# Kernel tuning notes

Hardware: AMD Instinct MI355X
Metric: run time of the kernel (lower is better)

## Reference

```python
import jax, jax.numpy as jnp
import numpy as np

N, M, P = 64, 64, 64
T = 262144

def setup_inputs() -> dict:
    key = jax.random.key(0)
    ks = jax.random.split(key, 6)
    return {
        "u": jax.random.normal(ks[0], (T, M), dtype=jnp.float32),
        "x0": jax.random.normal(ks[1], (N,), dtype=jnp.float32),
        "A": jax.random.normal(ks[2], (N, N), dtype=jnp.float32) * 0.1,
        "B": jax.random.normal(ks[3], (N, M), dtype=jnp.float32) * 0.1,
        "C": jax.random.normal(ks[4], (P, N), dtype=jnp.float32) * 0.1,
        "D": jax.random.normal(ks[5], (P, M), dtype=jnp.float32) * 0.1,
    }

def reference(u, x0, A, B, C, D):
    # Precompute input drives in one big GEMM each: Bu[k] = B @ u[k], Du[k] = D @ u[k]
    Bu = u @ B.T            # (T, n)
    Du = u @ D.T            # (T, p)

    def step(x, bu):
        # y_k uses pre-update state x_k; next state x_{k+1} = A x_k + B u_k
        x_next = A @ x + bu
        return x_next, x     # carry new state, emit x_k

    _, xs = jax.lax.scan(step, x0, Bu)   # xs: (T, n) = [x_0 ... x_{T-1}]
    ys = xs @ C.T + Du                   # (T, p)
    return ys
```

## Files before the change

### kernel.cpp

```cpp
#include <hip/hip_runtime.h>


#define T_LEN  262144
#define NTAP   33
#define ZLEN   48
#define ROWS   512
#define HALO   32

typedef __attribute__((ext_vector_type(8))) short  short8;
typedef __attribute__((ext_vector_type(4))) short  short4v;
typedef __attribute__((ext_vector_type(4))) float  floatx4;

static __device__ __forceinline__ unsigned short f2bf(float f) {
    unsigned int x = __float_as_uint(f);
    x += 0x7fffu + ((x >> 16) & 1u);
    return (unsigned short)(x >> 16);
}
static __device__ __forceinline__ float bf2f(unsigned short u) {
    return __uint_as_float(((unsigned int)u) << 16);
}

__global__ __launch_bounds__(256, 1) void k_prep(
    const float* __restrict__ A, const float* __restrict__ B,
    const float* __restrict__ C, const float* __restrict__ D,
    const float* __restrict__ x0, unsigned short* __restrict__ gG,
    float* __restrict__ gZ)
{
    __shared__ unsigned short pool[10][64][72];
    const int tid = threadIdx.x;
    const int wv = tid >> 6, lane = tid & 63, l15 = lane & 15, q = lane >> 4;

#pragma unroll
    for (int e = 0; e < 16; ++e) {
        int f = e * 256 + tid;
        int r = f >> 6, c = f & 63;
        unsigned short av = f2bf(A[f]);
        pool[0][r][c] = av;
        pool[1][c][r] = av;
        pool[2][c][r] = f2bf(B[f]);
        pool[6][r][c] = f2bf(C[f]);
        gG[f]         = f2bf(D[f]);
    }
    __syncthreads();

    float x0v[4];
#pragma unroll
    for (int nt = 0; nt < 4; ++nt) x0v[nt] = x0[l15 + 16 * nt];

    {
        short8 bA[2][4];
#pragma unroll
        for (int kb = 0; kb < 2; ++kb)
#pragma unroll
            for (int nt = 0; nt < 4; ++nt)
                bA[kb][nt] = *(const short8*)&pool[1][l15 + 16*nt][kb*32 + q*8];

        short8 a0 = *(const short8*)&pool[0][16*wv + l15][q*8];
        short8 a1 = *(const short8*)&pool[0][16*wv + l15][32 + q*8];
#pragma unroll
        for (int nt = 0; nt < 4; ++nt) {
            floatx4 m = (floatx4){0.f, 0.f, 0.f, 0.f};
            m = __builtin_amdgcn_mfma_f32_16x16x32_bf16(a0, bA[0][nt], m, 0, 0, 0);
            m = __builtin_amdgcn_mfma_f32_16x16x32_bf16(a1, bA[1][nt], m, 0, 0, 0);
#pragma unroll
            for (int r = 0; r < 4; ++r) {
                unsigned short h = f2bf(m[r]);
                pool[3][16*wv + q*4 + r][l15 + 16*nt] = h;
                pool[4][l15 + 16*nt][16*wv + q*4 + r] = h;
            }
        }
        a0 = *(const short8*)&pool[6][16*wv + l15][q*8];
        a1 = *(const short8*)&pool[6][16*wv + l15][32 + q*8];
#pragma unroll
        for (int nt = 0; nt < 4; ++nt) {
            floatx4 m = (floatx4){0.f, 0.f, 0.f, 0.f};
            m = __builtin_amdgcn_mfma_f32_16x16x32_bf16(a0, bA[0][nt], m, 0, 0, 0);
            m = __builtin_amdgcn_mfma_f32_16x16x32_bf16(a1, bA[1][nt], m, 0, 0, 0);
#pragma unroll
            for (int r = 0; r < 4; ++r)
                pool[7][16*wv + q*4 + r][l15 + 16*nt] = f2bf(m[r]);
        }
    }
    __syncthreads();

    {
        short8 bA2[2][4];
#pragma unroll
        for (int kb = 0; kb < 2; ++kb)
#pragma unroll
            for (int nt = 0; nt < 4; ++nt)
                bA2[kb][nt] = *(const short8*)&pool[4][l15 + 16*nt][kb*32 + q*8];

        short8 a0 = *(const short8*)&pool[3][16*wv + l15][q*8];
        short8 a1 = *(const short8*)&pool[3][16*wv + l15][32 + q*8];
#pragma unroll
        for (int nt = 0; nt < 4; ++nt) {
            floatx4 m = (floatx4){0.f, 0.f, 0.f, 0.f};
            m = __builtin_amdgcn_mfma_f32_16x16x32_bf16(a0, bA2[0][nt], m, 0, 0, 0);
            m = __builtin_amdgcn_mfma_f32_16x16x32_bf16(a1, bA2[1][nt], m, 0, 0, 0);
#pragma unroll
            for (int r = 0; r < 4; ++r)
                pool[5][l15 + 16*nt][16*wv + q*4 + r] = f2bf(m[r]);
        }
        a0 = *(const short8*)&pool[6][16*wv + l15][q*8];
        a1 = *(const short8*)&pool[6][16*wv + l15][32 + q*8];
#pragma unroll
        for (int nt = 0; nt < 4; ++nt) {
            floatx4 m = (floatx4){0.f, 0.f, 0.f, 0.f};
            m = __builtin_amdgcn_mfma_f32_16x16x32_bf16(a0, bA2[0][nt], m, 0, 0, 0);
            m = __builtin_amdgcn_mfma_f32_16x16x32_bf16(a1, bA2[1][nt], m, 0, 0, 0);
#pragma unroll
            for (int r = 0; r < 4; ++r)
                pool[8][16*wv + q*4 + r][l15 + 16*nt] = f2bf(m[r]);
        }
        a0 = *(const short8*)&pool[7][16*wv + l15][q*8];
        a1 = *(const short8*)&pool[7][16*wv + l15][32 + q*8];
#pragma unroll
        for (int nt = 0; nt < 4; ++nt) {
            floatx4 m = (floatx4){0.f, 0.f, 0.f, 0.f};
            m = __builtin_amdgcn_mfma_f32_16x16x32_bf16(a0, bA2[0][nt], m, 0, 0, 0);
            m = __builtin_amdgcn_mfma_f32_16x16x32_bf16(a1, bA2[1][nt], m, 0, 0, 0);
#pragma unroll
            for (int r = 0; r < 4; ++r)
                pool[9][16*wv + q*4 + r][l15 + 16*nt] = f2bf(m[r]);
        }
    }
    __syncthreads();

    short8 bE[2][4], bB[2][4];
#pragma unroll
    for (int kb = 0; kb < 2; ++kb)
#pragma unroll
        for (int nt = 0; nt < 4; ++nt) {
            bE[kb][nt] = *(const short8*)&pool[5][l15 + 16*nt][kb*32 + q*8];
            bB[kb][nt] = *(const short8*)&pool[2][l15 + 16*nt][kb*32 + q*8];
        }
    __syncthreads();

    unsigned short (*cur)[72] = pool[6 + wv];
    unsigned short (*alt)[72] = pool[wv];

#pragma unroll
    for (int mt = 0; mt < 4; ++mt)
#pragma unroll
        for (int r = 0; r < 4; ++r) {
            float v = 0.f;
#pragma unroll
            for (int nt = 0; nt < 4; ++nt)
                v += bf2f(cur[16*mt + q*4 + r][l15 + 16*nt]) * x0v[nt];
            v += __shfl_xor(v, 1, 16); v += __shfl_xor(v, 2, 16);
            v += __shfl_xor(v, 4, 16); v += __shfl_xor(v, 8, 16);
            if (l15 == 0) gZ[wv*64 + 16*mt + q*4 + r] = v;
        }

    for (int k = 1; k <= 11; ++k) {
        const int jm = 4*(k-1) + wv;
        short8 a0[4], a1[4];
#pragma unroll
        for (int mt = 0; mt < 4; ++mt) {
            a0[mt] = *(const short8*)&cur[16*mt + l15][q*8];
            a1[mt] = *(const short8*)&cur[16*mt + l15][32 + q*8];
        }
        if (jm < 32) {
#pragma unroll
            for (int mt = 0; mt < 4; ++mt)
#pragma unroll
                for (int nt = 0; nt < 4; ++nt) {
                    floatx4 g = (floatx4){0.f, 0.f, 0.f, 0.f};
                    g = __builtin_amdgcn_mfma_f32_16x16x32_bf16(a0[mt], bB[0][nt], g, 0, 0, 0);
                    g = __builtin_amdgcn_mfma_f32_16x16x32_bf16(a1[mt], bB[1][nt], g, 0, 0, 0);
#pragma unroll
                    for (int r = 0; r < 4; ++r)
                        gG[(size_t)(jm+1)*4096 + (16*mt + q*4 + r)*64 + l15 + 16*nt] = f2bf(g[r]);
                }
        }
        floatx4 m[4][4];
#pragma unroll
        for (int mt = 0; mt < 4; ++mt)
#pragma unroll
            for (int nt = 0; nt < 4; ++nt) {
                m[mt][nt] = (floatx4){0.f, 0.f, 0.f, 0.f};
                m[mt][nt] = __builtin_amdgcn_mfma_f32_16x16x32_bf16(a0[mt], bE[0][nt], m[mt][nt], 0, 0, 0);
                m[mt][nt] = __builtin_amdgcn_mfma_f32_16x16x32_bf16(a1[mt], bE[1][nt], m[mt][nt], 0, 0, 0);
            }
#pragma unroll
        for (int mt = 0; mt < 4; ++mt)
#pragma unroll
            for (int nt = 0; nt < 4; ++nt)
#pragma unroll
                for (int r = 0; r < 4; ++r)
                    alt[16*mt + q*4 + r][l15 + 16*nt] = f2bf(m[mt][nt][r]);
        const int zi = 4*k + wv;
#pragma unroll
        for (int mt = 0; mt < 4; ++mt)
#pragma unroll
            for (int r = 0; r < 4; ++r) {
                float v = 0.f;
#pragma unroll
                for (int nt = 0; nt < 4; ++nt) v = fmaf(m[mt][nt][r], x0v[nt], v);
                v += __shfl_xor(v, 1, 16); v += __shfl_xor(v, 2, 16);
                v += __shfl_xor(v, 4, 16); v += __shfl_xor(v, 8, 16);
                if (l15 == 0) gZ[zi*64 + 16*mt + q*4 + r] = v;
            }
        unsigned short (*tmp)[72] = cur; cur = alt; alt = tmp;
    }
}

__global__ __launch_bounds__(512, 2) void k_conv(
    const float* __restrict__ u, const unsigned short* __restrict__ gG,
    const float* __restrict__ gZ, float* __restrict__ out)
{
    __shared__ __align__(16) unsigned char uS[(ROWS + HALO) * 128];
    const int tid = threadIdx.x;
    const int wv = tid >> 6, lane = tid & 63, l15 = lane & 15, q = lane >> 4;
    const int nhalf = wv & 1, rg = wv >> 1;
    const int t0 = blockIdx.x * ROWS;

    {
        const float4* u4 = (const float4*)u;
        const int base4 = (t0 - HALO) * 16;
#pragma unroll
        for (int e = 0; e < 17; ++e) {
            int f = e * 512 + tid;
            float4 v = make_float4(0.f, 0.f, 0.f, 0.f);
            if (base4 + f >= 0) v = u4[base4 + f];
            int r  = f >> 4;
            int cb = (f & 15) * 8;
            short4v pk;
            pk[0] = (short)f2bf(v.x); pk[1] = (short)f2bf(v.y);
            pk[2] = (short)f2bf(v.z); pk[3] = (short)f2bf(v.w);
            *(short4v*)(uS + (r * 128 + (cb ^ ((r & 7) << 4)))) = pk;
        }
    }
    __syncthreads();

    floatx4 acc[8][2];
#pragma unroll
    for (int mt = 0; mt < 8; ++mt)
#pragma unroll
        for (int nt = 0; nt < 2; ++nt) acc[mt][nt] = (floatx4){0.f, 0.f, 0.f, 0.f};

    auto loadG2 = [&](short8 (&c0)[2][2], short8 (&c1)[2][2], int j) {
#pragma unroll
        for (int kb = 0; kb < 2; ++kb)
#pragma unroll
            for (int nt = 0; nt < 2; ++nt) {
                const size_t off = (size_t)(l15 + 16*(2*nhalf + nt))*64 + kb*32 + q*8;
                c1[kb][nt] = *(const short8*)(gG + (size_t)(j + 16)*4096 + off);
                c0[kb][nt] = *(const short8*)(gG + (size_t)j*4096 + off);
            }
    };
    auto sweep = [&](const short8 (&c0)[2][2], const short8 (&c1)[2][2], int j) {
        const int swz  = ((l15 - j) & 7) << 4;
        const int rowb = (rg*128 + 16 - j + l15) * 128;
        const int cb0 = (q * 16) ^ swz;
        const int cb1 = (64 + q * 16) ^ swz;
        short8 av[9], bv[9];
#pragma unroll
        for (int rt = 0; rt <= 8; ++rt)
            av[rt] = *(const short8*)(uS + (rowb + rt * 2048 + cb0));
#pragma unroll
        for (int rt = 0; rt <= 8; ++rt)
            bv[rt] = *(const short8*)(uS + (rowb + rt * 2048 + cb1));
#pragma unroll
        for (int rt = 0; rt <= 8; ++rt) {
            if (rt >= 1) {
#pragma unroll
                for (int nt = 0; nt < 2; ++nt)
                    acc[rt-1][nt] = __builtin_amdgcn_mfma_f32_16x16x32_bf16(
                        av[rt], c0[0][nt], acc[rt-1][nt], 0, 0, 0);
            }
            if (rt <= 7) {
#pragma unroll
                for (int nt = 0; nt < 2; ++nt)
                    acc[rt][nt] = __builtin_amdgcn_mfma_f32_16x16x32_bf16(
                        av[rt], c1[0][nt], acc[rt][nt], 0, 0, 0);
            }
        }
#pragma unroll
        for (int rt = 0; rt <= 8; ++rt) {
            if (rt >= 1) {
#pragma unroll
                for (int nt = 0; nt < 2; ++nt)
                    acc[rt-1][nt] = __builtin_amdgcn_mfma_f32_16x16x32_bf16(
                        bv[rt], c0[1][nt], acc[rt-1][nt], 0, 0, 0);
            }
            if (rt <= 7) {
#pragma unroll
                for (int nt = 0; nt < 2; ++nt)
                    acc[rt][nt] = __builtin_amdgcn_mfma_f32_16x16x32_bf16(
                        bv[rt], c1[1][nt], acc[rt][nt], 0, 0, 0);
            }
        }
    };

    short8 bA0[2][2], bA1[2][2], bB0[2][2], bB1[2][2];
    loadG2(bA0, bA1, 0);
#pragma unroll 1
    for (int jj = 0; jj < 8; ++jj) {
        loadG2(bB0, bB1, 2*jj + 1);
        sweep(bA0, bA1, 2*jj);
        if (jj < 7) loadG2(bA0, bA1, 2*jj + 2);
        sweep(bB0, bB1, 2*jj + 1);
    }

    {
        short8 bt[2][2];
#pragma unroll
        for (int kb = 0; kb < 2; ++kb)
#pragma unroll
            for (int nt = 0; nt < 2; ++nt)
                bt[kb][nt] = *(const short8*)(gG + (size_t)32*4096
                                  + (size_t)(l15 + 16*(2*nhalf + nt))*64 + kb*32 + q*8);
        const int swz  = (l15 & 7) << 4;
        const int rowb = (rg*128 + l15) * 128;
        const int cb0 = (q * 16) ^ swz;
        const int cb1 = (64 + q * 16) ^ swz;
        short8 av[8], bv[8];
#pragma unroll
        for (int mt = 0; mt < 8; ++mt)
            av[mt] = *(const short8*)(uS + (rowb + mt * 2048 + cb0));
#pragma unroll
        for (int mt = 0; mt < 8; ++mt)
            bv[mt] = *(const short8*)(uS + (rowb + mt * 2048 + cb1));
#pragma unroll
        for (int mt = 0; mt < 8; ++mt)
#pragma unroll
            for (int nt = 0; nt < 2; ++nt)
                acc[mt][nt] = __builtin_amdgcn_mfma_f32_16x16x32_bf16(
                    av[mt], bt[0][nt], acc[mt][nt], 0, 0, 0);
#pragma unroll
        for (int mt = 0; mt < 8; ++mt)
#pragma unroll
            for (int nt = 0; nt < 2; ++nt)
                acc[mt][nt] = __builtin_amdgcn_mfma_f32_16x16x32_bf16(
                    bv[mt], bt[1][nt], acc[mt][nt], 0, 0, 0);
    }

    const bool zblk = (blockIdx.x == 0 && rg == 0);
#pragma unroll
    for (int mt = 0; mt < 8; ++mt)
#pragma unroll
        for (int nt = 0; nt < 2; ++nt) {
            const int p = l15 + 32*nhalf + 16*nt;
#pragma unroll
            for (int r = 0; r < 4; ++r) {
                int tl = rg*128 + mt*16 + q*4 + r;
                float v = acc[mt][nt][r];
                if (zblk && mt < 3) v += gZ[(mt*16 + q*4 + r)*64 + p];
                out[(size_t)(t0 + tl)*64 + p] = v;
            }
        }
}

extern "C" void kernel_launch(void* const* d_in, const int* in_sizes, int n_in,
                              void* d_out, int out_size, void* d_ws, size_t ws_size,
                              hipStream_t stream) {
    const float* u  = (const float*)d_in[0];
    const float* x0 = (const float*)d_in[1];
    const float* A  = (const float*)d_in[2];
    const float* B  = (const float*)d_in[3];
    const float* C  = (const float*)d_in[4];
    const float* D  = (const float*)d_in[5];
    float* out = (float*)d_out;

    unsigned short* gG = (unsigned short*)d_ws;
    float* gZ = (float*)((char*)d_ws + 272384);

    hipLaunchKernelGGL(k_prep, dim3(1), dim3(256), 0, stream,
                       A, B, C, D, x0, gG, gZ);
    hipLaunchKernelGGL(k_conv, dim3(T_LEN / ROWS), dim3(512), 0, stream,
                       u, gG, gZ, out);
}
```

Baseline: 239.4 us.

## Pre-cast input to bf16 buffer and read operands directly from global memory

Adds a separate cast kernel that converts u to a zero-padded bf16 buffer in the workspace, then a new convolution kernel that reads MFMA operands straight from this buffer through the cache instead of staging fp32 input into swizzled LDS. Block size drops to 256 threads covering 256 rows. The aim is to remove the LDS staging and the fp32-to-bf16 conversion from the main kernel. In exchange it adds an extra launch plus a full write and re-read of a bf16 copy of u, and the halo rows are now loaded redundantly from global memory. The old LDS path remains as a fallback when the workspace is too small.

```diff
diff --git a/kernel.cpp b/kernel.cpp
--- a/kernel.cpp
+++ b/kernel.cpp
@@ -4,8 +4,8 @@
 #define T_LEN  262144
 #define NTAP   33
 #define ZLEN   48
-#define ROWS   512
 #define HALO   32
+#define UB_ROWS (T_LEN + HALO)
 
 typedef __attribute__((ext_vector_type(8))) short  short8;
 typedef __attribute__((ext_vector_type(4))) short  short4v;
@@ -18,6 +18,24 @@
 }
 static __device__ __forceinline__ float bf2f(unsigned short u) {
     return __uint_as_float(((unsigned int)u) << 16);
+}
+
+__global__ __launch_bounds__(256) void k_cast(
+    const float* __restrict__ u, unsigned short* __restrict__ uB)
+{
+    const size_t e8 = ((size_t)blockIdx.x * 256 + threadIdx.x) * 8;
+    short8 pk;
+    if (e8 < (size_t)HALO * 64) {
+        pk = (short8){0, 0, 0, 0, 0, 0, 0, 0};
+    } else {
+        const float4* s = (const float4*)(u + (e8 - (size_t)HALO * 64));
+        float4 v0 = s[0], v1 = s[1];
+        pk[0] = (short)f2bf(v0.x); pk[1] = (short)f2bf(v0.y);
+        pk[2] = (short)f2bf(v0.z); pk[3] = (short)f2bf(v0.w);
+        pk[4] = (short)f2bf(v1.x); pk[5] = (short)f2bf(v1.y);
+        pk[6] = (short)f2bf(v1.z); pk[7] = (short)f2bf(v1.w);
+    }
+    *(short8*)(uB + e8) = pk;
 }
 
 __global__ __launch_bounds__(256, 1) void k_prep(
@@ -206,7 +224,136 @@
     }
 }
 
-__global__ __launch_bounds__(512, 2) void k_conv(
+__global__ __launch_bounds__(256, 2) void k_conv_g(
+    const unsigned short* __restrict__ uB, const unsigned short* __restrict__ gG,
+    const float* __restrict__ gZ, float* __restrict__ out)
+{
+    const int tid = threadIdx.x;
+    const int wv = tid >> 6, lane = tid & 63, l15 = lane & 15, q = lane >> 4;
+    const int nhalf = wv & 1, rg = wv >> 1;
+    const int t0 = blockIdx.x * 256;
+    const unsigned char* uBb = (const unsigned char*)uB;
+
+    floatx4 acc[8][2];
+#pragma unroll
+    for (int mt = 0; mt < 8; ++mt)
+#pragma unroll
+        for (int nt = 0; nt < 2; ++nt) acc[mt][nt] = (floatx4){0.f, 0.f, 0.f, 0.f};
+
+    auto loadG2 = [&](short8 (&c0)[2][2], short8 (&c1)[2][2], int j) {
+#pragma unroll
+        for (int kb = 0; kb < 2; ++kb)
+#pragma unroll
+            for (int nt = 0; nt < 2; ++nt) {
+                const size_t off = (size_t)(l15 + 16*(2*nhalf + nt))*64 + kb*32 + q*8;
+                c1[kb][nt] = *(const short8*)(gG + (size_t)(j + 16)*4096 + off);
+                c0[kb][nt] = *(const short8*)(gG + (size_t)j*4096 + off);
+            }
+    };
+
+    const unsigned char* wbase = uBb + ((size_t)t0 + rg*128 + 16 + l15) * 128;
+    const int cb0 = q * 16;
+    const int cb1 = 64 + q * 16;
+
+    auto sweep = [&](const short8 (&c0)[2][2], const short8 (&c1)[2][2], int j) {
+        const unsigned char* rb = wbase - j * 128;
+        short8 av[9], bv[9];
+#pragma unroll
+        for (int rt = 0; rt <= 8; ++rt)
+            av[rt] = *(const short8*)(rb + rt * 2048 + cb0);
+#pragma unroll
+        for (int rt = 0; rt <= 8; ++rt)
+            bv[rt] = *(const short8*)(rb + rt * 2048 + cb1);
+#pragma unroll
+        for (int rt = 0; rt <= 8; ++rt) {
+            if (rt >= 1) {
+#pragma unroll
+                for (int nt = 0; nt < 2; ++nt)
+                    acc[rt-1][nt] = __builtin_amdgcn_mfma_f32_16x16x32_bf16(
+                        av[rt], c0[0][nt], acc[rt-1][nt], 0, 0, 0);
+            }
+            if (rt <= 7) {
+#pragma unroll
+                for (int nt = 0; nt < 2; ++nt)
+                    acc[rt][nt] = __builtin_amdgcn_mfma_f32_16x16x32_bf16(
+                        av[rt], c1[0][nt], acc[rt][nt], 0, 0, 0);
+            }
+        }
+#pragma unroll
+        for (int rt = 0; rt <= 8; ++rt) {
+            if (rt >= 1) {
+#pragma unroll
+                for (int nt = 0; nt < 2; ++nt)
+                    acc[rt-1][nt] = __builtin_amdgcn_mfma_f32_16x16x32_bf16(
+                        bv[rt], c0[1][nt], acc[rt-1][nt], 0, 0, 0);
+            }
+            if (rt <= 7) {
+#pragma unroll
+                for (int nt = 0; nt < 2; ++nt)
+                    acc[rt][nt] = __builtin_amdgcn_mfma_f32_16x16x32_bf16(
+                        bv[rt], c1[1][nt], acc[rt][nt], 0, 0, 0);
+            }
+        }
+    };
+
+    short8 bA0[2][2], bA1[2][2], bB0[2][2], bB1[2][2];
+    loadG2(bA0, bA1, 0);
+#pragma unroll 1
+    for (int jj = 0; jj < 8; ++jj) {
+        loadG2(bB0, bB1, 2*jj + 1);
+        sweep(bA0, bA1, 2*jj);
+        if (jj < 7) loadG2(bA0, bA1, 2*jj + 2);
+        sweep(bB0, bB1, 2*jj + 1);
+    }
+
+    {
+        short8 bt[2][2];
+#pragma unroll
+        for (int kb = 0; kb < 2; ++kb)
+#pragma unroll
+            for (int nt = 0; nt < 2; ++nt)
+                bt[kb][nt] = *(const short8*)(gG + (size_t)32*4096
+                                  + (size_t)(l15 + 16*(2*nhalf + nt))*64 + kb*32 + q*8);
+        const unsigned char* rb = uBb + ((size_t)t0 + rg*128 + l15) * 128;
+        short8 av[8], bv[8];
+#pragma unroll
+        for (int mt = 0; mt < 8; ++mt)
+            av[mt] = *(const short8*)(rb + mt * 2048 + cb0);
+#pragma unroll
+        for (int mt = 0; mt < 8; ++mt)
+            bv[mt] = *(const short8*)(rb + mt * 2048 + cb1);
+#pragma unroll
+        for (int mt = 0; mt < 8; ++mt)
+#pragma unroll
+            for (int nt = 0; nt < 2; ++nt)
+                acc[mt][nt] = __builtin_amdgcn_mfma_f32_16x16x32_bf16(
+                    av[mt], bt[0][nt], acc[mt][nt], 0, 0, 0);
+#pragma unroll
+        for (int mt = 0; mt < 8; ++mt)
+#pragma unroll
+            for (int nt = 0; nt < 2; ++nt)
+                acc[mt][nt] = __builtin_amdgcn_mfma_f32_16x16x32_bf16(
+                    bv[mt], bt[1][nt], acc[mt][nt], 0, 0, 0);
+    }
+
+    const bool zblk = (blockIdx.x == 0 && rg == 0);
+#pragma unroll
+    for (int mt = 0; mt < 8; ++mt)
+#pragma unroll
+        for (int nt = 0; nt < 2; ++nt) {
+            const int p = l15 + 32*nhalf + 16*nt;
+#pragma unroll
+            for (int r = 0; r < 4; ++r) {
+                int tl = rg*128 + mt*16 + q*4 + r;
+                float v = acc[mt][nt][r];
+                if (zblk && mt < 3) v += gZ[(mt*16 + q*4 + r)*64 + p];
+                out[(size_t)(t0 + tl)*64 + p] = v;
+            }
+        }
+}
+
+#define ROWS 512
+__global__ __launch_bounds__(512, 2) void k_conv_lds(
     const float* __restrict__ u, const unsigned short* __restrict__ gG,
     const float* __restrict__ gZ, float* __restrict__ out)
 {
@@ -303,7 +450,6 @@
         if (jj < 7) loadG2(bA0, bA1, 2*jj + 2);
         sweep(bB0, bB1, 2*jj + 1);
     }
-
     {
         short8 bt[2][2];
 #pragma unroll
@@ -336,7 +482,6 @@
                 acc[mt][nt] = __builtin_amdgcn_mfma_f32_16x16x32_bf16(
                     bv[mt], bt[1][nt], acc[mt][nt], 0, 0, 0);
     }
-
     const bool zblk = (blockIdx.x == 0 && rg == 0);
 #pragma unroll
     for (int mt = 0; mt < 8; ++mt)
@@ -366,9 +511,18 @@
 
     unsigned short* gG = (unsigned short*)d_ws;
     float* gZ = (float*)((char*)d_ws + 272384);
+    unsigned short* uB = (unsigned short*)((char*)d_ws + 284672);
+    const size_t need = 284672 + (size_t)UB_ROWS * 64 * sizeof(unsigned short);
 
     hipLaunchKernelGGL(k_prep, dim3(1), dim3(256), 0, stream,
                        A, B, C, D, x0, gG, gZ);
-    hipLaunchKernelGGL(k_conv, dim3(T_LEN / ROWS), dim3(512), 0, stream,
-                       u, gG, gZ, out);
-}
+    if (ws_size >= need) {
+        hipLaunchKernelGGL(k_cast, dim3((UB_ROWS * 64 / 8 + 255) / 256), dim3(256),
+                           0, stream, u, uB);
+        hipLaunchKernelGGL(k_conv_g, dim3(T_LEN / 256), dim3(256), 0, stream,
+                           uB, gG, gZ, out);
+    } else {
+        hipLaunchKernelGGL(k_conv_lds, dim3(T_LEN / ROWS), dim3(512), 0, stream,
+                           u, gG, gZ, out);
+    }
+}
```

Result: slower. 361.7 us (+51.1%).
